# Performance work log

Measured on AMD Instinct MI355X. Metric: run time of the kernel, lower is better.

Reference implementation:

```python
import jax, jax.numpy as jnp
import numpy as np
import math

B, N, D = 16, 2048, 256

def setup_inputs() -> dict:
    key = jax.random.key(0)
    kq, kk, kv = jax.random.split(key, 3)
    query = jax.random.normal(kq, (B, N, D), dtype=jnp.float32)
    k = jax.random.normal(kk, (B, N, D), dtype=jnp.float32)
    value = jax.random.normal(kv, (B, D, N), dtype=jnp.float32)  # channel-first [B, d_v, N]
    return {"query": query, "key": k, "value": value, "mask": 0}

def reference(query, key, value, mask):
    d_k = query.shape[-1]
    scale = 1.0 / math.sqrt(d_k)
    # scores: [B, N, N]
    scores = jnp.einsum('bnd,bmd->bnm', query, key) * scale
    p_attn = jax.nn.softmax(scores, axis=-1)
    # mask is a static Python int flag gating dropout; mask=0 -> no dropout (deterministic reference)
    if mask:
        pass  # dropout intentionally disabled in deterministic reference
    # out = p_attn @ value^T  -> [B, N, d_v]; module returns out.transpose(-2,-1) -> [B, d_v, N]
    out_t = jnp.einsum('bnm,bdm->bdn', p_attn, value)
    return (out_t, p_attn)
```

## Files before the change

kernel.cpp:

```cpp
#include <hip/hip_runtime.h>
#include <hip/hip_bf16.h>


using bf16x8 = __attribute__((ext_vector_type(8))) short;
using f32x4  = __attribute__((ext_vector_type(4))) float;

__device__ __forceinline__ short f2bf(float f) {
    unsigned u = __float_as_uint(f);
    u += 0x7fffu + ((u >> 16) & 1u);
    return (short)(u >> 16);
}

__device__ __forceinline__ f32x4 mfma16(bf16x8 a, bf16x8 b, f32x4 c) {
    return __builtin_amdgcn_mfma_f32_16x16x32_bf16(a, b, c, 0, 0, 0);
}

#define AS1(p) ((const __attribute__((address_space(1))) void*)(p))
#define AS3(p) ((__attribute__((address_space(3))) void*)(p))

__global__ __launch_bounds__(256)
void convert_qkv(const float* __restrict__ Q, const float* __restrict__ K,
                 const float* __restrict__ V, short* __restrict__ Qb,
                 short* __restrict__ Kb, short* __restrict__ Vb, size_t n8)
{
    size_t i = (size_t)blockIdx.x * 256 + threadIdx.x;
    const float* src;
    short* dst;
    float scale = 1.0f;
    if (i < n8)            { src = Q;  dst = Qb; scale = 0.0625f; }
    else if (i < 2 * n8)   { i -= n8;      src = K; dst = Kb; }
    else                   { i -= 2 * n8;  src = V; dst = Vb; }
    const f32x4* s4 = (const f32x4*)src;
    f32x4 a = __builtin_nontemporal_load(s4 + i * 2);
    f32x4 b = __builtin_nontemporal_load(s4 + i * 2 + 1);
    bf16x8 v;
    v[0] = f2bf(a[0] * scale); v[1] = f2bf(a[1] * scale);
    v[2] = f2bf(a[2] * scale); v[3] = f2bf(a[3] * scale);
    v[4] = f2bf(b[0] * scale); v[5] = f2bf(b[1] * scale);
    v[6] = f2bf(b[2] * scale); v[7] = f2bf(b[3] * scale);
    *(bf16x8*)(dst + i * 8) = v;
}

__global__ __launch_bounds__(512, 2)
void fused_attn(const short* __restrict__ Qb, const short* __restrict__ Kb,
                const short* __restrict__ Vb, float* __restrict__ Pout,
                float* __restrict__ outT)
{
    __shared__ __align__(16) short Klds[2][64 * 256];
    __shared__ __align__(16) short Vlds[2][256 * 64];
    __shared__ __align__(16) short Plds[128 * 64];
    float* lpart = (float*)Plds;

    constexpr float LOG2E = 1.4426950408889634f;

    const unsigned g  = blockIdx.x;
    const unsigned wg = (g & 7) * 32 + (g >> 3);
    const int b  = (int)(wg >> 4);
    const int nb = (int)(wg & 15);

    const int tid  = threadIdx.x;
    const int lane = tid & 63;
    const int wave = tid >> 6;
    const int wn  = wave >> 1;
    const int wm  = wave & 1;
    const int l15 = lane & 15;
    const int l4  = lane >> 4;

    const short* Kbase = Kb + (size_t)b * (2048 * 256);
    const short* Vbase = Vb + (size_t)b * (256 * 2048);

    const short* Qp = Qb + ((size_t)b * 2048 + (size_t)nb * 128) * 256;
    bf16x8 qf[2][8];
#pragma unroll
    for (int mf = 0; mf < 2; mf++)
#pragma unroll
        for (int ks = 0; ks < 8; ks++)
            qf[mf][ks] = *(const bf16x8*)(
                Qp + (size_t)(wn * 32 + mf * 16 + l15) * 256 + ks * 32 + l4 * 8);

    auto stage_k = [&](int t, int buf) {
#pragma unroll
        for (int i = 0; i < 4; i++) {
            int ml = i * 16 + wave * 2 + (lane >> 5);
            int c  = lane & 31;
            int cs = (c & 24) | ((c ^ ml) & 7);
            __builtin_amdgcn_global_load_lds(
                AS1(Kbase + (size_t)(t * 64 + ml) * 256 + cs * 8),
                AS3(&Klds[buf][i * 4096 + wave * 512]), 16, 0, 0);
        }
    };
    auto stage_v = [&](int t, int buf) {
#pragma unroll
        for (int i = 0; i < 4; i++) {
            int d  = i * 64 + wave * 8 + (lane >> 3);
            int c  = lane & 7;
            int cs = c ^ (d & 7);
            __builtin_amdgcn_global_load_lds(
                AS1(Vbase + (size_t)d * 2048 + t * 64 + cs * 8),
                AS3(&Vlds[buf][i * 4096 + wave * 512]), 16, 0, 0);
        }
    };

    auto qkt = [&](int buf, f32x4 sacT[2][2]) {
#pragma unroll
        for (int ks = 0; ks < 8; ks++) {
            bf16x8 kf[2];
#pragma unroll
            for (int nf = 0; nf < 2; nf++) {
                int m  = wm * 32 + nf * 16 + l15;
                int ch = (ks * 4 + l4) ^ (m & 7);
                kf[nf] = *(const bf16x8*)((const char*)&Klds[buf][0] + m * 512 + ch * 16);
            }
#pragma unroll
            for (int mf = 0; mf < 2; mf++)
#pragma unroll
                for (int nf = 0; nf < 2; nf++)
                    sacT[mf][nf] = mfma16(kf[nf], qf[mf][ks], sacT[mf][nf]);
        }
    };

    float lacc[2] = {0.f, 0.f};
    stage_k(0, 0);
    for (int t = 0; t < 32; t++) {
        __syncthreads();
        if (t + 1 < 32) stage_k(t + 1, (t + 1) & 1);
        f32x4 sacT[2][2];
#pragma unroll
        for (int mf = 0; mf < 2; mf++)
#pragma unroll
            for (int nf = 0; nf < 2; nf++)
                sacT[mf][nf] = f32x4{0.f, 0.f, 0.f, 0.f};
        qkt(t & 1, sacT);
#pragma unroll
        for (int mf = 0; mf < 2; mf++)
#pragma unroll
            for (int nf = 0; nf < 2; nf++)
#pragma unroll
                for (int r = 0; r < 4; r++)
                    lacc[mf] += exp2f(sacT[mf][nf][r] * LOG2E);
    }
#pragma unroll
    for (int mf = 0; mf < 2; mf++) {
        lacc[mf] += __shfl_xor(lacc[mf], 16);
        lacc[mf] += __shfl_xor(lacc[mf], 32);
    }
    if (l4 == 0) {
        lpart[wave * 32 + 0 * 16 + l15] = lacc[0];
        lpart[wave * 32 + 1 * 16 + l15] = lacc[1];
    }
    __syncthreads();
    float rl[2];
#pragma unroll
    for (int mf = 0; mf < 2; mf++)
        rl[mf] = 1.0f / (lpart[(wn * 2 + 0) * 32 + mf * 16 + l15] +
                         lpart[(wn * 2 + 1) * 32 + mf * 16 + l15]);

    f32x4 oac[4][4];
#pragma unroll
    for (int i = 0; i < 4; i++)
#pragma unroll
        for (int j = 0; j < 4; j++)
            oac[i][j] = f32x4{0.f, 0.f, 0.f, 0.f};

    stage_k(0, 0);
    stage_v(0, 0);
    float* prow = Pout + ((size_t)b * 2048 + (size_t)nb * 128) * 2048;

    for (int t = 0; t < 32; t++) {
        __syncthreads();
        f32x4 sacT[2][2];
#pragma unroll
        for (int mf = 0; mf < 2; mf++)
#pragma unroll
            for (int nf = 0; nf < 2; nf++)
                sacT[mf][nf] = f32x4{0.f, 0.f, 0.f, 0.f};
        qkt(t & 1, sacT);

        f32x4 pv4[2][2];
#pragma unroll
        for (int mf = 0; mf < 2; mf++)
#pragma unroll
            for (int nf = 0; nf < 2; nf++) {
#pragma unroll
                for (int r = 0; r < 4; r++)
                    pv4[mf][nf][r] = exp2f(sacT[mf][nf][r] * LOG2E) * rl[mf];
                short4 ps;
                ps.x = f2bf(pv4[mf][nf][0]); ps.y = f2bf(pv4[mf][nf][1]);
                ps.z = f2bf(pv4[mf][nf][2]); ps.w = f2bf(pv4[mf][nf][3]);
                const int n  = wn * 32 + mf * 16 + l15;
                const int mb = wm * 32 + nf * 16 + l4 * 4;
                const int ch = (mb >> 3) ^ (n & 7);
                *(short4*)((char*)Plds + n * 128 + ch * 16 + (mb & 7) * 2) = ps;
            }
        __syncthreads();

        if (t + 1 < 32) {
            stage_k(t + 1, (t + 1) & 1);
            stage_v(t + 1, (t + 1) & 1);
        }

#pragma unroll
        for (int mf = 0; mf < 2; mf++)
#pragma unroll
            for (int nf = 0; nf < 2; nf++) {
                const int n  = wn * 32 + mf * 16 + l15;
                const int m  = t * 64 + wm * 32 + nf * 16 + l4 * 4;
                __builtin_nontemporal_store(pv4[mf][nf],
                    (f32x4*)(prow + (size_t)n * 2048 + m));
            }

        const char* vb_ = (const char*)&Vlds[t & 1][0];
#pragma unroll
        for (int ksl = 0; ksl < 2; ksl++) {
            bf16x8 vf[4], pf[4];
#pragma unroll
            for (int mf4 = 0; mf4 < 4; mf4++) {
                const int d  = wn * 64 + mf4 * 16 + l15;
                const int ch = (ksl * 4 + l4) ^ (d & 7);
                vf[mf4] = *(const bf16x8*)(vb_ + d * 128 + ch * 16);
            }
#pragma unroll
            for (int nf4 = 0; nf4 < 4; nf4++) {
                const int n  = wm * 64 + nf4 * 16 + l15;
                const int ch = (ksl * 4 + l4) ^ (n & 7);
                pf[nf4] = *(const bf16x8*)((const char*)Plds + n * 128 + ch * 16);
            }
#pragma unroll
            for (int mf4 = 0; mf4 < 4; mf4++)
#pragma unroll
                for (int nf4 = 0; nf4 < 4; nf4++)
                    oac[mf4][nf4] = mfma16(vf[mf4], pf[nf4], oac[mf4][nf4]);
        }
    }

    float* op = outT + (size_t)b * (256 * 2048) + (size_t)nb * 128;
#pragma unroll
    for (int mf4 = 0; mf4 < 4; mf4++)
#pragma unroll
        for (int nf4 = 0; nf4 < 4; nf4++)
#pragma unroll
            for (int r = 0; r < 4; r++) {
                int d = wn * 64 + mf4 * 16 + l4 * 4 + r;
                int n = wm * 64 + nf4 * 16 + l15;
                op[(size_t)d * 2048 + n] = oac[mf4][nf4][r];
            }
}

template<int BM, int BN, int BK>
__global__ __launch_bounds__(256)
void gemm_abt(const float* __restrict__ A, const float* __restrict__ B,
              float* __restrict__ C, int M, int N, int K,
              long strideA, long strideB, long strideC, float scale)
{
    const int b  = blockIdx.z;
    const int bm = blockIdx.y;
    const int bn = blockIdx.x;
    A += (size_t)b * strideA;
    B += (size_t)b * strideB;
    C += (size_t)b * strideC;

    constexpr int LDT = BK + 8;
    __shared__ __align__(16) short Alds[BM][LDT];
    __shared__ __align__(16) short Blds[BN][LDT];

    const int tid  = threadIdx.x;
    const int lane = tid & 63;
    const int wave = tid >> 6;
    const int wr   = wave >> 1;
    const int wc   = wave & 1;

    f32x4 acc[4][4];
#pragma unroll
    for (int m = 0; m < 4; m++)
#pragma unroll
        for (int n = 0; n < 4; n++)
            acc[m][n] = f32x4{0.f, 0.f, 0.f, 0.f};

    const float* Ab = A + (size_t)(bm * BM) * K;
    const float* Bb = B + (size_t)(bn * BN) * K;

    const int tr  = tid >> 4;
    const int tc4 = (tid & 15) << 2;

    for (int k0 = 0; k0 < K; k0 += BK) {
        __syncthreads();
#pragma unroll
        for (int r = tr; r < BM; r += 16) {
            const float4 v = *(const float4*)(Ab + (size_t)r * K + k0 + tc4);
            short4 s;
            s.x = f2bf(v.x); s.y = f2bf(v.y); s.z = f2bf(v.z); s.w = f2bf(v.w);
            *(short4*)&Alds[r][tc4] = s;
        }
#pragma unroll
        for (int r = tr; r < BN; r += 16) {
            const float4 v = *(const float4*)(Bb + (size_t)r * K + k0 + tc4);
            short4 s;
            s.x = f2bf(v.x); s.y = f2bf(v.y); s.z = f2bf(v.z); s.w = f2bf(v.w);
            *(short4*)&Blds[r][tc4] = s;
        }
        __syncthreads();

#pragma unroll
        for (int kk = 0; kk < BK; kk += 32) {
            const int ko = kk + ((lane >> 4) << 3);
            bf16x8 af[4], bfr[4];
#pragma unroll
            for (int m = 0; m < 4; m++)
                af[m] = *(const bf16x8*)&Alds[wr * 64 + m * 16 + (lane & 15)][ko];
#pragma unroll
            for (int n = 0; n < 4; n++)
                bfr[n] = *(const bf16x8*)&Blds[wc * 64 + n * 16 + (lane & 15)][ko];
#pragma unroll
            for (int m = 0; m < 4; m++)
#pragma unroll
                for (int n = 0; n < 4; n++)
                    acc[m][n] = __builtin_amdgcn_mfma_f32_16x16x32_bf16(
                        af[m], bfr[n], acc[m][n], 0, 0, 0);
        }
    }

    float* Cb = C + (size_t)(bm * BM) * N + (size_t)bn * BN;
    const int rbase = wr * 64 + ((lane >> 4) << 2);
    const int cbase = wc * 64 + (lane & 15);
#pragma unroll
    for (int m = 0; m < 4; m++)
#pragma unroll
        for (int n = 0; n < 4; n++)
#pragma unroll
            for (int r = 0; r < 4; r++)
                Cb[(size_t)(rbase + m * 16 + r) * N + cbase + n * 16] =
                    acc[m][n][r] * scale;
}

__global__ __launch_bounds__(256)
void softmax_rows(float* __restrict__ P)
{
    const size_t row = blockIdx.x;
    float* p = P + row * 2048;
    const int tid  = threadIdx.x;
    const int lane = tid & 63;
    const int wave = tid >> 6;

    float4 v0 = ((const float4*)p)[tid];
    float4 v1 = ((const float4*)p)[tid + 256];

    float m = fmaxf(fmaxf(fmaxf(v0.x, v0.y), fmaxf(v0.z, v0.w)),
                    fmaxf(fmaxf(v1.x, v1.y), fmaxf(v1.z, v1.w)));
#pragma unroll
    for (int off = 32; off; off >>= 1) m = fmaxf(m, __shfl_xor(m, off));

    __shared__ float sred[4];
    __shared__ float ssum[4];
    if (lane == 0) sred[wave] = m;
    __syncthreads();
    m = fmaxf(fmaxf(sred[0], sred[1]), fmaxf(sred[2], sred[3]));

    v0.x = expf(v0.x - m); v0.y = expf(v0.y - m);
    v0.z = expf(v0.z - m); v0.w = expf(v0.w - m);
    v1.x = expf(v1.x - m); v1.y = expf(v1.y - m);
    v1.z = expf(v1.z - m); v1.w = expf(v1.w - m);

    float s = (v0.x + v0.y + v0.z + v0.w) + (v1.x + v1.y + v1.z + v1.w);
#pragma unroll
    for (int off = 32; off; off >>= 1) s += __shfl_xor(s, off);
    if (lane == 0) ssum[wave] = s;
    __syncthreads();
    s = ssum[0] + ssum[1] + ssum[2] + ssum[3];

    const float r = 1.0f / s;
    v0.x *= r; v0.y *= r; v0.z *= r; v0.w *= r;
    v1.x *= r; v1.y *= r; v1.z *= r; v1.w *= r;

    ((float4*)p)[tid]       = v0;
    ((float4*)p)[tid + 256] = v1;
}

extern "C" void kernel_launch(void* const* d_in, const int* in_sizes, int n_in,
                              void* d_out, int out_size, void* d_ws, size_t ws_size,
                              hipStream_t stream)
{
    const float* Q  = (const float*)d_in[0];
    const float* Kk = (const float*)d_in[1];
    const float* V  = (const float*)d_in[2];

    float* outT = (float*)d_out;
    float* P    = outT + (size_t)16 * 256 * 2048;

    const size_t nQ = (size_t)16 * 2048 * 256;
    const long sQK = (long)2048 * 256;
    const long sP  = (long)2048 * 2048;
    const long sO  = (long)256 * 2048;

    const size_t needQKV = 3 * nQ * sizeof(short);

    if (ws_size >= needQKV) {
        short* Qb = (short*)d_ws;
        short* Kb = Qb + nQ;
        short* Vb = Kb + nQ;

        convert_qkv<<<dim3((unsigned)(3 * nQ / 8 / 256)), 256, 0, stream>>>(
            Q, Kk, V, Qb, Kb, Vb, nQ / 8);

        fused_attn<<<dim3(256), 512, 0, stream>>>(Qb, Kb, Vb, P, outT);
    } else {
        gemm_abt<128, 128, 64><<<dim3(16, 16, 16), 256, 0, stream>>>(
            Q, Kk, P, 2048, 2048, 256, sQK, sQK, sP, 0.0625f);
        softmax_rows<<<dim3(16 * 2048), 256, 0, stream>>>(P);
        gemm_abt<128, 128, 64><<<dim3(16, 2, 16), 256, 0, stream>>>(
            V, P, outT, 256, 2048, 2048, sO, sP, sO, 1.0f);
    }
}
```

Before: 185.1 us.

## Halve query tile to 64 rows, single-buffer V in LDS, raise occupancy

The fused attention kernel now gives each block 64 query rows instead of 128 and launches 512 blocks instead of 256. K and V are no longer double-buffered in the second pass; they share one LDS region, and launch bounds ask for 4 blocks per CU. Per-wave accumulators shrink, and s_setprio is raised around the MFMA sections. The aim is more resident waves and better CU fill for hiding latency, at the cost of recomputing QK^T for twice as many blocks, reloading K/V twice as often, and giving up load/compute overlap in the second pass.

```diff
diff --git a/kernel.cpp b/kernel.cpp
--- a/kernel.cpp
+++ b/kernel.cpp
@@ -41,35 +41,36 @@
     *(bf16x8*)(dst + i * 8) = v;
 }
 
-__global__ __launch_bounds__(512, 2)
+__global__ __launch_bounds__(512, 4)
 void fused_attn(const short* __restrict__ Qb, const short* __restrict__ Kb,
                 const short* __restrict__ Vb, float* __restrict__ Pout,
                 float* __restrict__ outT)
 {
-    __shared__ __align__(16) short Klds[2][64 * 256];
-    __shared__ __align__(16) short Vlds[2][256 * 64];
-    __shared__ __align__(16) short Plds[128 * 64];
+    __shared__ __align__(16) short Kl[2][64 * 256];
+    __shared__ __align__(16) short Plds[64 * 64];
     float* lpart = (float*)Plds;
 
     constexpr float LOG2E = 1.4426950408889634f;
 
     const unsigned g  = blockIdx.x;
-    const unsigned wg = (g & 7) * 32 + (g >> 3);
-    const int b  = (int)(wg >> 4);
-    const int nb = (int)(wg & 15);
+    const unsigned wg = (g & 7) * 64 + (g >> 3);
+    const int b  = (int)(wg >> 5);
+    const int nb = (int)(wg & 31);
 
     const int tid  = threadIdx.x;
     const int lane = tid & 63;
     const int wave = tid >> 6;
-    const int wn  = wave >> 1;
-    const int wm  = wave & 1;
     const int l15 = lane & 15;
     const int l4  = lane >> 4;
+    const int wn  = wave & 1;
+    const int wm  = wave >> 1;
+    const int nh  = wave & 1;
+    const int dq  = wave >> 1;
 
     const short* Kbase = Kb + (size_t)b * (2048 * 256);
     const short* Vbase = Vb + (size_t)b * (256 * 2048);
 
-    const short* Qp = Qb + ((size_t)b * 2048 + (size_t)nb * 128) * 256;
+    const short* Qp = Qb + ((size_t)b * 2048 + (size_t)nb * 64) * 256;
     bf16x8 qf[2][8];
 #pragma unroll
     for (int mf = 0; mf < 2; mf++)
@@ -86,10 +87,10 @@
             int cs = (c & 24) | ((c ^ ml) & 7);
             __builtin_amdgcn_global_load_lds(
                 AS1(Kbase + (size_t)(t * 64 + ml) * 256 + cs * 8),
-                AS3(&Klds[buf][i * 4096 + wave * 512]), 16, 0, 0);
+                AS3(&Kl[buf][i * 4096 + wave * 512]), 16, 0, 0);
         }
     };
-    auto stage_v = [&](int t, int buf) {
+    auto stage_v = [&](int t) {
 #pragma unroll
         for (int i = 0; i < 4; i++) {
             int d  = i * 64 + wave * 8 + (lane >> 3);
@@ -97,26 +98,22 @@
             int cs = c ^ (d & 7);
             __builtin_amdgcn_global_load_lds(
                 AS1(Vbase + (size_t)d * 2048 + t * 64 + cs * 8),
-                AS3(&Vlds[buf][i * 4096 + wave * 512]), 16, 0, 0);
+                AS3(&Kl[1][i * 4096 + wave * 512]), 16, 0, 0);
         }
     };
 
-    auto qkt = [&](int buf, f32x4 sacT[2][2]) {
+    auto qkt = [&](int buf, f32x4 sacT[2]) {
+        __builtin_amdgcn_s_setprio(1);
 #pragma unroll
         for (int ks = 0; ks < 8; ks++) {
-            bf16x8 kf[2];
-#pragma unroll
-            for (int nf = 0; nf < 2; nf++) {
-                int m  = wm * 32 + nf * 16 + l15;
-                int ch = (ks * 4 + l4) ^ (m & 7);
-                kf[nf] = *(const bf16x8*)((const char*)&Klds[buf][0] + m * 512 + ch * 16);
-            }
+            const int m  = wm * 16 + l15;
+            const int ch = (ks * 4 + l4) ^ (m & 7);
+            bf16x8 kf = *(const bf16x8*)((const char*)&Kl[buf][0] + m * 512 + ch * 16);
 #pragma unroll
             for (int mf = 0; mf < 2; mf++)
-#pragma unroll
-                for (int nf = 0; nf < 2; nf++)
-                    sacT[mf][nf] = mfma16(kf[nf], qf[mf][ks], sacT[mf][nf]);
-        }
+                sacT[mf] = mfma16(kf, qf[mf][ks], sacT[mf]);
+        }
+        __builtin_amdgcn_s_setprio(0);
     };
 
     float lacc[2] = {0.f, 0.f};
@@ -124,20 +121,15 @@
     for (int t = 0; t < 32; t++) {
         __syncthreads();
         if (t + 1 < 32) stage_k(t + 1, (t + 1) & 1);
-        f32x4 sacT[2][2];
+        f32x4 sacT[2];
+        sacT[0] = f32x4{0.f, 0.f, 0.f, 0.f};
+        sacT[1] = f32x4{0.f, 0.f, 0.f, 0.f};
+        qkt(t & 1, sacT);
 #pragma unroll
         for (int mf = 0; mf < 2; mf++)
 #pragma unroll
-            for (int nf = 0; nf < 2; nf++)
-                sacT[mf][nf] = f32x4{0.f, 0.f, 0.f, 0.f};
-        qkt(t & 1, sacT);
-#pragma unroll
-        for (int mf = 0; mf < 2; mf++)
-#pragma unroll
-            for (int nf = 0; nf < 2; nf++)
-#pragma unroll
-                for (int r = 0; r < 4; r++)
-                    lacc[mf] += exp2f(sacT[mf][nf][r] * LOG2E);
+            for (int r = 0; r < 4; r++)
+                lacc[mf] += exp2f(sacT[mf][r] * LOG2E);
     }
 #pragma unroll
     for (int mf = 0; mf < 2; mf++) {
@@ -151,98 +143,98 @@
     __syncthreads();
     float rl[2];
 #pragma unroll
-    for (int mf = 0; mf < 2; mf++)
-        rl[mf] = 1.0f / (lpart[(wn * 2 + 0) * 32 + mf * 16 + l15] +
-                         lpart[(wn * 2 + 1) * 32 + mf * 16 + l15]);
-
-    f32x4 oac[4][4];
+    for (int mf = 0; mf < 2; mf++) {
+        float s = 0.f;
+#pragma unroll
+        for (int w4 = 0; w4 < 4; w4++)
+            s += lpart[(w4 * 2 + wn) * 32 + mf * 16 + l15];
+        rl[mf] = 1.0f / s;
+    }
+    __syncthreads();
+
+    f32x4 oac[4][2];
 #pragma unroll
     for (int i = 0; i < 4; i++)
 #pragma unroll
-        for (int j = 0; j < 4; j++)
+        for (int j = 0; j < 2; j++)
             oac[i][j] = f32x4{0.f, 0.f, 0.f, 0.f};
 
     stage_k(0, 0);
-    stage_v(0, 0);
-    float* prow = Pout + ((size_t)b * 2048 + (size_t)nb * 128) * 2048;
+    stage_v(0);
+    float* prow = Pout + ((size_t)b * 2048 + (size_t)nb * 64) * 2048;
 
     for (int t = 0; t < 32; t++) {
         __syncthreads();
-        f32x4 sacT[2][2];
-#pragma unroll
-        for (int mf = 0; mf < 2; mf++)
-#pragma unroll
-            for (int nf = 0; nf < 2; nf++)
-                sacT[mf][nf] = f32x4{0.f, 0.f, 0.f, 0.f};
-        qkt(t & 1, sacT);
-
-        f32x4 pv4[2][2];
-#pragma unroll
-        for (int mf = 0; mf < 2; mf++)
-#pragma unroll
-            for (int nf = 0; nf < 2; nf++) {
-#pragma unroll
-                for (int r = 0; r < 4; r++)
-                    pv4[mf][nf][r] = exp2f(sacT[mf][nf][r] * LOG2E) * rl[mf];
-                short4 ps;
-                ps.x = f2bf(pv4[mf][nf][0]); ps.y = f2bf(pv4[mf][nf][1]);
-                ps.z = f2bf(pv4[mf][nf][2]); ps.w = f2bf(pv4[mf][nf][3]);
-                const int n  = wn * 32 + mf * 16 + l15;
-                const int mb = wm * 32 + nf * 16 + l4 * 4;
-                const int ch = (mb >> 3) ^ (n & 7);
-                *(short4*)((char*)Plds + n * 128 + ch * 16 + (mb & 7) * 2) = ps;
+        f32x4 sacT[2];
+        sacT[0] = f32x4{0.f, 0.f, 0.f, 0.f};
+        sacT[1] = f32x4{0.f, 0.f, 0.f, 0.f};
+        qkt(0, sacT);
+
+        f32x4 pv4[2];
+#pragma unroll
+        for (int mf = 0; mf < 2; mf++) {
+#pragma unroll
+            for (int r = 0; r < 4; r++)
+                pv4[mf][r] = exp2f(sacT[mf][r] * LOG2E) * rl[mf];
+            short4 ps;
+            ps.x = f2bf(pv4[mf][0]); ps.y = f2bf(pv4[mf][1]);
+            ps.z = f2bf(pv4[mf][2]); ps.w = f2bf(pv4[mf][3]);
+            const int n  = wn * 32 + mf * 16 + l15;
+            const int mb = wm * 16 + l4 * 4;
+            const int ch = (mb >> 3) ^ (n & 7);
+            *(short4*)((char*)Plds + n * 128 + ch * 16 + (mb & 7) * 2) = ps;
+        }
+        __syncthreads();
+
+#pragma unroll
+        for (int mf = 0; mf < 2; mf++) {
+            const int n = wn * 32 + mf * 16 + l15;
+            const int m = t * 64 + wm * 16 + l4 * 4;
+            __builtin_nontemporal_store(pv4[mf],
+                (f32x4*)(prow + (size_t)n * 2048 + m));
+        }
+
+        __builtin_amdgcn_s_setprio(1);
+#pragma unroll
+        for (int ksl = 0; ksl < 2; ksl++) {
+            bf16x8 vf[4], pf[2];
+#pragma unroll
+            for (int mf4 = 0; mf4 < 4; mf4++) {
+                const int d  = dq * 64 + mf4 * 16 + l15;
+                const int ch = (ksl * 4 + l4) ^ (d & 7);
+                vf[mf4] = *(const bf16x8*)((const char*)&Kl[1][0] + d * 128 + ch * 16);
             }
+#pragma unroll
+            for (int nf2 = 0; nf2 < 2; nf2++) {
+                const int n  = nh * 32 + nf2 * 16 + l15;
+                const int ch = (ksl * 4 + l4) ^ (n & 7);
+                pf[nf2] = *(const bf16x8*)((const char*)Plds + n * 128 + ch * 16);
+            }
+#pragma unroll
+            for (int mf4 = 0; mf4 < 4; mf4++)
+#pragma unroll
+                for (int nf2 = 0; nf2 < 2; nf2++)
+                    oac[mf4][nf2] = mfma16(vf[mf4], pf[nf2], oac[mf4][nf2]);
+        }
+        __builtin_amdgcn_s_setprio(0);
         __syncthreads();
 
         if (t + 1 < 32) {
-            stage_k(t + 1, (t + 1) & 1);
-            stage_v(t + 1, (t + 1) & 1);
-        }
-
-#pragma unroll
-        for (int mf = 0; mf < 2; mf++)
-#pragma unroll
-            for (int nf = 0; nf < 2; nf++) {
-                const int n  = wn * 32 + mf * 16 + l15;
-                const int m  = t * 64 + wm * 32 + nf * 16 + l4 * 4;
-                __builtin_nontemporal_store(pv4[mf][nf],
-                    (f32x4*)(prow + (size_t)n * 2048 + m));
-            }
-
-        const char* vb_ = (const char*)&Vlds[t & 1][0];
-#pragma unroll
-        for (int ksl = 0; ksl < 2; ksl++) {
-            bf16x8 vf[4], pf[4];
-#pragma unroll
-            for (int mf4 = 0; mf4 < 4; mf4++) {
-                const int d  = wn * 64 + mf4 * 16 + l15;
-                const int ch = (ksl * 4 + l4) ^ (d & 7);
-                vf[mf4] = *(const bf16x8*)(vb_ + d * 128 + ch * 16);
-            }
-#pragma unroll
-            for (int nf4 = 0; nf4 < 4; nf4++) {
-                const int n  = wm * 64 + nf4 * 16 + l15;
-                const int ch = (ksl * 4 + l4) ^ (n & 7);
-                pf[nf4] = *(const bf16x8*)((const char*)Plds + n * 128 + ch * 16);
-            }
-#pragma unroll
-            for (int mf4 = 0; mf4 < 4; mf4++)
-#pragma unroll
-                for (int nf4 = 0; nf4 < 4; nf4++)
-                    oac[mf4][nf4] = mfma16(vf[mf4], pf[nf4], oac[mf4][nf4]);
-        }
-    }
-
-    float* op = outT + (size_t)b * (256 * 2048) + (size_t)nb * 128;
+            stage_k(t + 1, 0);
+            stage_v(t + 1);
+        }
+    }
+
+    float* op = outT + (size_t)b * (256 * 2048) + (size_t)nb * 64;
 #pragma unroll
     for (int mf4 = 0; mf4 < 4; mf4++)
 #pragma unroll
-        for (int nf4 = 0; nf4 < 4; nf4++)
+        for (int nf2 = 0; nf2 < 2; nf2++)
 #pragma unroll
             for (int r = 0; r < 4; r++) {
-                int d = wn * 64 + mf4 * 16 + l4 * 4 + r;
-                int n = wm * 64 + nf4 * 16 + l15;
-                op[(size_t)d * 2048 + n] = oac[mf4][nf4][r];
+                int d = dq * 64 + mf4 * 16 + l4 * 4 + r;
+                int n = nh * 32 + nf2 * 16 + l15;
+                op[(size_t)d * 2048 + n] = oac[mf4][nf2][r];
             }
 }
 
@@ -401,7 +393,7 @@
         convert_qkv<<<dim3((unsigned)(3 * nQ / 8 / 256)), 256, 0, stream>>>(
             Q, Kk, V, Qb, Kb, Vb, nQ / 8);
 
-        fused_attn<<<dim3(256), 512, 0, stream>>>(Qb, Kb, Vb, P, outT);
+        fused_attn<<<dim3(512), 512, 0, stream>>>(Qb, Kb, Vb, P, outT);
     } else {
         gemm_abt<128, 128, 64><<<dim3(16, 16, 16), 256, 0, stream>>>(
             Q, Kk, P, 2048, 2048, 256, sQK, sQK, sP, 0.0625f);
```

Measured after the change: 380.7 us. +105.7%, slower.

## Warp-specialize attention: producer waves compute P, consumer waves do PV

Applied to the files above, without the earlier changes.

The second pass of the fused attention kernel is split by role. Waves 0-3 compute the QK^T tile, the softmax probabilities and the P global stores. Waves 4-7 run the P·V^T MFMAs for the previous tile, reading from a now double-buffered P in LDS, so only one barrier is needed per iteration. V staging is issued one step earlier, K for the second pass is prefetched during the normalizer reduction, and s_setprio raises wave priority around the MFMA loops. This aims to overlap the exp/store work with the PV matrix math, at the cost of 160KB of LDS, more accumulator registers in the consumer waves and a pipeline that can only go as fast as its slower half.

```diff
diff --git a/kernel.cpp b/kernel.cpp
--- a/kernel.cpp
+++ b/kernel.cpp
@@ -46,10 +46,10 @@
                 const short* __restrict__ Vb, float* __restrict__ Pout,
                 float* __restrict__ outT)
 {
-    __shared__ __align__(16) short Klds[2][64 * 256];
-    __shared__ __align__(16) short Vlds[2][256 * 64];
-    __shared__ __align__(16) short Plds[128 * 64];
-    float* lpart = (float*)Plds;
+    __shared__ __align__(16) short Kl[2][64 * 256];
+    __shared__ __align__(16) short Vl[2][256 * 64];
+    __shared__ __align__(16) short Pl[2][128 * 64];
+    float* lpart = (float*)Pl;
 
     constexpr float LOG2E = 1.4426950408889634f;
 
@@ -61,10 +61,9 @@
     const int tid  = threadIdx.x;
     const int lane = tid & 63;
     const int wave = tid >> 6;
-    const int wn  = wave >> 1;
-    const int wm  = wave & 1;
     const int l15 = lane & 15;
     const int l4  = lane >> 4;
+    const int qg  = wave & 3;
 
     const short* Kbase = Kb + (size_t)b * (2048 * 256);
     const short* Vbase = Vb + (size_t)b * (256 * 2048);
@@ -76,7 +75,7 @@
 #pragma unroll
         for (int ks = 0; ks < 8; ks++)
             qf[mf][ks] = *(const bf16x8*)(
-                Qp + (size_t)(wn * 32 + mf * 16 + l15) * 256 + ks * 32 + l4 * 8);
+                Qp + (size_t)(qg * 32 + mf * 16 + l15) * 256 + ks * 32 + l4 * 8);
 
     auto stage_k = [&](int t, int buf) {
 #pragma unroll
@@ -86,7 +85,7 @@
             int cs = (c & 24) | ((c ^ ml) & 7);
             __builtin_amdgcn_global_load_lds(
                 AS1(Kbase + (size_t)(t * 64 + ml) * 256 + cs * 8),
-                AS3(&Klds[buf][i * 4096 + wave * 512]), 16, 0, 0);
+                AS3(&Kl[buf][i * 4096 + wave * 512]), 16, 0, 0);
         }
     };
     auto stage_v = [&](int t, int buf) {
@@ -97,25 +96,7 @@
             int cs = c ^ (d & 7);
             __builtin_amdgcn_global_load_lds(
                 AS1(Vbase + (size_t)d * 2048 + t * 64 + cs * 8),
-                AS3(&Vlds[buf][i * 4096 + wave * 512]), 16, 0, 0);
-        }
-    };
-
-    auto qkt = [&](int buf, f32x4 sacT[2][2]) {
-#pragma unroll
-        for (int ks = 0; ks < 8; ks++) {
-            bf16x8 kf[2];
-#pragma unroll
-            for (int nf = 0; nf < 2; nf++) {
-                int m  = wm * 32 + nf * 16 + l15;
-                int ch = (ks * 4 + l4) ^ (m & 7);
-                kf[nf] = *(const bf16x8*)((const char*)&Klds[buf][0] + m * 512 + ch * 16);
-            }
-#pragma unroll
-            for (int mf = 0; mf < 2; mf++)
-#pragma unroll
-                for (int nf = 0; nf < 2; nf++)
-                    sacT[mf][nf] = mfma16(kf[nf], qf[mf][ks], sacT[mf][nf]);
+                AS3(&Vl[buf][i * 4096 + wave * 512]), 16, 0, 0);
         }
     };
 
@@ -124,13 +105,30 @@
     for (int t = 0; t < 32; t++) {
         __syncthreads();
         if (t + 1 < 32) stage_k(t + 1, (t + 1) & 1);
+        const char* kbuf = (const char*)&Kl[t & 1][0];
         f32x4 sacT[2][2];
 #pragma unroll
         for (int mf = 0; mf < 2; mf++)
 #pragma unroll
             for (int nf = 0; nf < 2; nf++)
                 sacT[mf][nf] = f32x4{0.f, 0.f, 0.f, 0.f};
-        qkt(t & 1, sacT);
+        __builtin_amdgcn_s_setprio(1);
+#pragma unroll
+        for (int ks = 0; ks < 8; ks++) {
+            bf16x8 kf[2];
+#pragma unroll
+            for (int nf = 0; nf < 2; nf++) {
+                int m  = (wave >> 2) * 32 + nf * 16 + l15;
+                int ch = (ks * 4 + l4) ^ (m & 7);
+                kf[nf] = *(const bf16x8*)(kbuf + m * 512 + ch * 16);
+            }
+#pragma unroll
+            for (int mf = 0; mf < 2; mf++)
+#pragma unroll
+                for (int nf = 0; nf < 2; nf++)
+                    sacT[mf][nf] = mfma16(kf[nf], qf[mf][ks], sacT[mf][nf]);
+        }
+        __builtin_amdgcn_s_setprio(0);
 #pragma unroll
         for (int mf = 0; mf < 2; mf++)
 #pragma unroll
@@ -139,6 +137,7 @@
                 for (int r = 0; r < 4; r++)
                     lacc[mf] += exp2f(sacT[mf][nf][r] * LOG2E);
     }
+    stage_k(0, 0);
 #pragma unroll
     for (int mf = 0; mf < 2; mf++) {
         lacc[mf] += __shfl_xor(lacc[mf], 16);
@@ -152,98 +151,114 @@
     float rl[2];
 #pragma unroll
     for (int mf = 0; mf < 2; mf++)
-        rl[mf] = 1.0f / (lpart[(wn * 2 + 0) * 32 + mf * 16 + l15] +
-                         lpart[(wn * 2 + 1) * 32 + mf * 16 + l15]);
-
-    f32x4 oac[4][4];
+        rl[mf] = 1.0f / (lpart[qg * 32 + mf * 16 + l15] +
+                         lpart[(qg + 4) * 32 + mf * 16 + l15]);
+    __syncthreads();
+
+    f32x4 oac[4][8];
 #pragma unroll
     for (int i = 0; i < 4; i++)
 #pragma unroll
-        for (int j = 0; j < 4; j++)
+        for (int j = 0; j < 8; j++)
             oac[i][j] = f32x4{0.f, 0.f, 0.f, 0.f};
 
-    stage_k(0, 0);
-    stage_v(0, 0);
     float* prow = Pout + ((size_t)b * 2048 + (size_t)nb * 128) * 2048;
+    const int cw = wave - 4;
+
+    auto consume = [&](int tt) {
+        const char* vbuf = (const char*)&Vl[tt & 1][0];
+        const char* pbuf = (const char*)&Pl[tt & 1][0];
+        __builtin_amdgcn_s_setprio(1);
+#pragma unroll
+        for (int ksl = 0; ksl < 2; ksl++) {
+            bf16x8 vf[4];
+#pragma unroll
+            for (int df = 0; df < 4; df++) {
+                int d  = cw * 64 + df * 16 + l15;
+                int ch = (ksl * 4 + l4) ^ (d & 7);
+                vf[df] = *(const bf16x8*)(vbuf + d * 128 + ch * 16);
+            }
+#pragma unroll
+            for (int nf = 0; nf < 8; nf++) {
+                int n  = nf * 16 + l15;
+                int ch = (ksl * 4 + l4) ^ (n & 7);
+                bf16x8 pf = *(const bf16x8*)(pbuf + n * 128 + ch * 16);
+#pragma unroll
+                for (int df = 0; df < 4; df++)
+                    oac[df][nf] = mfma16(vf[df], pf, oac[df][nf]);
+            }
+        }
+        __builtin_amdgcn_s_setprio(0);
+    };
 
     for (int t = 0; t < 32; t++) {
+        if (t + 1 < 32) stage_k(t + 1, (t + 1) & 1);
+        stage_v(t, t & 1);
+
+        if (wave < 4) {
+            const char* kbuf = (const char*)&Kl[t & 1][0];
+            f32x4 sacT[2][4];
+#pragma unroll
+            for (int mf = 0; mf < 2; mf++)
+#pragma unroll
+                for (int nf = 0; nf < 4; nf++)
+                    sacT[mf][nf] = f32x4{0.f, 0.f, 0.f, 0.f};
+            __builtin_amdgcn_s_setprio(1);
+#pragma unroll
+            for (int ks = 0; ks < 8; ks++) {
+                bf16x8 kf[4];
+#pragma unroll
+                for (int nf = 0; nf < 4; nf++) {
+                    int m  = nf * 16 + l15;
+                    int ch = (ks * 4 + l4) ^ (m & 7);
+                    kf[nf] = *(const bf16x8*)(kbuf + m * 512 + ch * 16);
+                }
+#pragma unroll
+                for (int mf = 0; mf < 2; mf++)
+#pragma unroll
+                    for (int nf = 0; nf < 4; nf++)
+                        sacT[mf][nf] = mfma16(kf[nf], qf[mf][ks], sacT[mf][nf]);
+            }
+            __builtin_amdgcn_s_setprio(0);
+
+            char* pw = (char*)&Pl[t & 1][0];
+#pragma unroll
+            for (int mf = 0; mf < 2; mf++)
+#pragma unroll
+                for (int nf = 0; nf < 4; nf++) {
+                    f32x4 pv4;
+#pragma unroll
+                    for (int r = 0; r < 4; r++)
+                        pv4[r] = exp2f(sacT[mf][nf][r] * LOG2E) * rl[mf];
+                    short4 ps;
+                    ps.x = f2bf(pv4[0]); ps.y = f2bf(pv4[1]);
+                    ps.z = f2bf(pv4[2]); ps.w = f2bf(pv4[3]);
+                    const int n  = qg * 32 + mf * 16 + l15;
+                    const int mb = nf * 16 + l4 * 4;
+                    const int ch = (mb >> 3) ^ (n & 7);
+                    *(short4*)(pw + n * 128 + ch * 16 + (mb & 7) * 2) = ps;
+                    __builtin_nontemporal_store(pv4,
+                        (f32x4*)(prow + (size_t)n * 2048 + t * 64 + mb));
+                }
+        } else if (t > 0) {
+            consume(t - 1);
+        }
         __syncthreads();
-        f32x4 sacT[2][2];
-#pragma unroll
-        for (int mf = 0; mf < 2; mf++)
-#pragma unroll
-            for (int nf = 0; nf < 2; nf++)
-                sacT[mf][nf] = f32x4{0.f, 0.f, 0.f, 0.f};
-        qkt(t & 1, sacT);
-
-        f32x4 pv4[2][2];
-#pragma unroll
-        for (int mf = 0; mf < 2; mf++)
-#pragma unroll
-            for (int nf = 0; nf < 2; nf++) {
-#pragma unroll
-                for (int r = 0; r < 4; r++)
-                    pv4[mf][nf][r] = exp2f(sacT[mf][nf][r] * LOG2E) * rl[mf];
-                short4 ps;
-                ps.x = f2bf(pv4[mf][nf][0]); ps.y = f2bf(pv4[mf][nf][1]);
-                ps.z = f2bf(pv4[mf][nf][2]); ps.w = f2bf(pv4[mf][nf][3]);
-                const int n  = wn * 32 + mf * 16 + l15;
-                const int mb = wm * 32 + nf * 16 + l4 * 4;
-                const int ch = (mb >> 3) ^ (n & 7);
-                *(short4*)((char*)Plds + n * 128 + ch * 16 + (mb & 7) * 2) = ps;
-            }
-        __syncthreads();
-
-        if (t + 1 < 32) {
-            stage_k(t + 1, (t + 1) & 1);
-            stage_v(t + 1, (t + 1) & 1);
-        }
-
-#pragma unroll
-        for (int mf = 0; mf < 2; mf++)
-#pragma unroll
-            for (int nf = 0; nf < 2; nf++) {
-                const int n  = wn * 32 + mf * 16 + l15;
-                const int m  = t * 64 + wm * 32 + nf * 16 + l4 * 4;
-                __builtin_nontemporal_store(pv4[mf][nf],
-                    (f32x4*)(prow + (size_t)n * 2048 + m));
-            }
-
-        const char* vb_ = (const char*)&Vlds[t & 1][0];
-#pragma unroll
-        for (int ksl = 0; ksl < 2; ksl++) {
-            bf16x8 vf[4], pf[4];
-#pragma unroll
-            for (int mf4 = 0; mf4 < 4; mf4++) {
-                const int d  = wn * 64 + mf4 * 16 + l15;
-                const int ch = (ksl * 4 + l4) ^ (d & 7);
-                vf[mf4] = *(const bf16x8*)(vb_ + d * 128 + ch * 16);
-            }
-#pragma unroll
-            for (int nf4 = 0; nf4 < 4; nf4++) {
-                const int n  = wm * 64 + nf4 * 16 + l15;
-                const int ch = (ksl * 4 + l4) ^ (n & 7);
-                pf[nf4] = *(const bf16x8*)((const char*)Plds + n * 128 + ch * 16);
-            }
-#pragma unroll
-            for (int mf4 = 0; mf4 < 4; mf4++)
-#pragma unroll
-                for (int nf4 = 0; nf4 < 4; nf4++)
-                    oac[mf4][nf4] = mfma16(vf[mf4], pf[nf4], oac[mf4][nf4]);
-        }
-    }
-
-    float* op = outT + (size_t)b * (256 * 2048) + (size_t)nb * 128;
-#pragma unroll
-    for (int mf4 = 0; mf4 < 4; mf4++)
-#pragma unroll
-        for (int nf4 = 0; nf4 < 4; nf4++)
-#pragma unroll
-            for (int r = 0; r < 4; r++) {
-                int d = wn * 64 + mf4 * 16 + l4 * 4 + r;
-                int n = wm * 64 + nf4 * 16 + l15;
-                op[(size_t)d * 2048 + n] = oac[mf4][nf4][r];
-            }
+    }
+    if (wave >= 4) {
+        consume(31);
+        float* op = outT + (size_t)b * (256 * 2048) + (size_t)nb * 128;
+#pragma unroll
+        for (int df = 0; df < 4; df++)
+#pragma unroll
+            for (int nf = 0; nf < 8; nf++)
+#pragma unroll
+                for (int r = 0; r < 4; r++) {
+                    int d = cw * 64 + df * 16 + l4 * 4 + r;
+                    int n = nf * 16 + l15;
+                    op[(size_t)d * 2048 + n] = oac[df][nf][r];
+                }
+    }
 }
 
 template<int BM, int BN, int BK>
```

Result: slower. 224.9 us (+21.5%).

## Split fused attention into a score GEMM and a fused softmax-PV kernel

Applied to the files above, without the earlier changes.

Replaces the single fused attention kernel, when workspace allows, with two kernels. The first is a tiled QK^T GEMM that stores bf16 scores and per-tile partial exp row sums. The second reads the scores, forms normalized probabilities, writes P, and multiplies by V with double-buffered LDS staging. This removes the in-kernel recomputation and serial dependency of the fused softmax and gives the GEMM much more parallelism, at the cost of a large bf16 score round trip through memory. The softmax skips max subtraction, which assumes the scaled scores stay small enough not to overflow exp.

```diff
diff --git a/kernel.cpp b/kernel.cpp
--- a/kernel.cpp
+++ b/kernel.cpp
@@ -10,13 +10,17 @@
     u += 0x7fffu + ((u >> 16) & 1u);
     return (short)(u >> 16);
 }
-
+__device__ __forceinline__ float bf2f(short s) {
+    return __uint_as_float(((unsigned)(unsigned short)s) << 16);
+}
 __device__ __forceinline__ f32x4 mfma16(bf16x8 a, bf16x8 b, f32x4 c) {
     return __builtin_amdgcn_mfma_f32_16x16x32_bf16(a, b, c, 0, 0, 0);
 }
 
 #define AS1(p) ((const __attribute__((address_space(1))) void*)(p))
 #define AS3(p) ((__attribute__((address_space(3))) void*)(p))
+
+constexpr float LOG2E = 1.4426950408889634f;
 
 __global__ __launch_bounds__(256)
 void convert_qkv(const float* __restrict__ Q, const float* __restrict__ K,
@@ -41,6 +45,247 @@
     *(bf16x8*)(dst + i * 8) = v;
 }
 
+__global__ __launch_bounds__(256)
+void gemm_s_lp(const short* __restrict__ A, const short* __restrict__ B,
+               short* __restrict__ Sb, float* __restrict__ lp)
+{
+    constexpr int BK = 64;
+    const unsigned g  = blockIdx.x;
+    const unsigned wg = (g & 7) * 512 + (g >> 3);
+    const int bn = (int)(wg & 15);
+    const int bm = (int)((wg >> 4) & 15);
+    const int b  = (int)(wg >> 8);
+
+    const short* Ab = A + (size_t)b * (2048 * 256) + (size_t)(bm * 128) * 256;
+    const short* Bb = B + (size_t)b * (2048 * 256) + (size_t)(bn * 128) * 256;
+
+    __shared__ __align__(16) short Alds[128 * BK];
+    __shared__ __align__(16) short Blds[128 * BK];
+    __shared__ float lred[2][128];
+
+    const int tid  = threadIdx.x;
+    const int lane = tid & 63;
+    const int wave = tid >> 6;
+    const int wr   = wave >> 1;
+    const int wc   = wave & 1;
+    const int l15  = lane & 15;
+    const int l4   = lane >> 4;
+
+    f32x4 acc[4][4];
+#pragma unroll
+    for (int m = 0; m < 4; m++)
+#pragma unroll
+        for (int n = 0; n < 4; n++)
+            acc[m][n] = f32x4{0.f, 0.f, 0.f, 0.f};
+
+    const int r0 = wave * 8 + (lane >> 3);
+    const int c0 = (lane & 7) * 8;
+
+    for (int k0 = 0; k0 < 256; k0 += BK) {
+        __syncthreads();
+#pragma unroll
+        for (int i = 0; i < 4; i++)
+            __builtin_amdgcn_global_load_lds(
+                AS1(Ab + (size_t)(i * 32 + r0) * 256 + k0 + c0),
+                AS3(Alds + i * 2048 + wave * 512), 16, 0, 0);
+#pragma unroll
+        for (int i = 0; i < 4; i++)
+            __builtin_amdgcn_global_load_lds(
+                AS1(Bb + (size_t)(i * 32 + r0) * 256 + k0 + c0),
+                AS3(Blds + i * 2048 + wave * 512), 16, 0, 0);
+        __syncthreads();
+
+#pragma unroll
+        for (int kk = 0; kk < BK; kk += 32) {
+            const int ko = kk + (l4 << 3);
+            bf16x8 af[4], bfr[4];
+#pragma unroll
+            for (int m = 0; m < 4; m++)
+                af[m] = *(const bf16x8*)&Alds[(wr * 64 + m * 16 + l15) * BK + ko];
+#pragma unroll
+            for (int n = 0; n < 4; n++)
+                bfr[n] = *(const bf16x8*)&Blds[(wc * 64 + n * 16 + l15) * BK + ko];
+#pragma unroll
+            for (int m = 0; m < 4; m++)
+#pragma unroll
+                for (int n = 0; n < 4; n++)
+                    acc[m][n] = mfma16(af[m], bfr[n], acc[m][n]);
+        }
+    }
+
+    short* Cb = Sb + (size_t)b * (2048UL * 2048) + (size_t)(bm * 128) * 2048
+              + (size_t)bn * 128;
+    const int rbase = wr * 64 + (l4 << 2);
+    const int cbase = wc * 64 + l15;
+    float esum[4][4];
+#pragma unroll
+    for (int m = 0; m < 4; m++)
+#pragma unroll
+        for (int r = 0; r < 4; r++)
+            esum[m][r] = 0.f;
+#pragma unroll
+    for (int m = 0; m < 4; m++)
+#pragma unroll
+        for (int n = 0; n < 4; n++)
+#pragma unroll
+            for (int r = 0; r < 4; r++) {
+                const short sv = f2bf(acc[m][n][r]);
+                Cb[(size_t)(rbase + m * 16 + r) * 2048 + cbase + n * 16] = sv;
+                esum[m][r] += exp2f(bf2f(sv) * LOG2E);
+            }
+#pragma unroll
+    for (int dlt = 1; dlt < 16; dlt <<= 1)
+#pragma unroll
+        for (int m = 0; m < 4; m++)
+#pragma unroll
+            for (int r = 0; r < 4; r++)
+                esum[m][r] += __shfl_xor(esum[m][r], dlt);
+    if (l15 == 0)
+#pragma unroll
+        for (int m = 0; m < 4; m++)
+#pragma unroll
+            for (int r = 0; r < 4; r++)
+                lred[wc][rbase + m * 16 + r] = esum[m][r];
+    __syncthreads();
+    if (tid < 128)
+        lp[((size_t)b * 2048 + bm * 128 + tid) * 16 + bn] =
+            lred[0][tid] + lred[1][tid];
+}
+
+__global__ __launch_bounds__(512, 2)
+void pv_attn(const short* __restrict__ Sb, const short* __restrict__ Vb,
+             const float* __restrict__ lp, float* __restrict__ Pout,
+             float* __restrict__ outT)
+{
+    __shared__ __align__(16) short Sl[2][128 * 64];
+    __shared__ __align__(16) short Vl[2][256 * 64];
+
+    const unsigned g  = blockIdx.x;
+    const unsigned wg = (g & 7) * 32 + (g >> 3);
+    const int b  = (int)(wg >> 4);
+    const int nb = (int)(wg & 15);
+
+    const int tid  = threadIdx.x;
+    const int lane = tid & 63;
+    const int wave = tid >> 6;
+    const int l15  = lane & 15;
+    const int l4   = lane >> 4;
+
+    const short* Sbase = Sb + ((size_t)b * 2048 + (size_t)nb * 128) * 2048;
+    const short* Vbase = Vb + (size_t)b * (256 * 2048);
+
+    const int nmine = tid >> 2;
+    const int mseg  = tid & 3;
+    const f32x4* lp4 = (const f32x4*)(lp + ((size_t)b * 2048 + nb * 128 + nmine) * 16);
+    float ls = 0.f;
+#pragma unroll
+    for (int j = 0; j < 4; j++) {
+        const f32x4 lv = lp4[j];
+        ls += lv[0] + lv[1] + lv[2] + lv[3];
+    }
+    const float rlmine = 1.0f / ls;
+    float* prow_mine = Pout + ((size_t)b * 2048 + (size_t)nb * 128 + nmine) * 2048;
+
+    auto stage_s = [&](int t, int buf) {
+#pragma unroll
+        for (int i = 0; i < 2; i++) {
+            int ri = i * 64 + wave * 8 + (lane >> 3);
+            int c  = lane & 7;
+            int cs = c ^ (ri & 7);
+            __builtin_amdgcn_global_load_lds(
+                AS1(Sbase + (size_t)ri * 2048 + t * 64 + cs * 8),
+                AS3(&Sl[buf][i * 4096 + wave * 512]), 16, 0, 0);
+        }
+    };
+    auto stage_v = [&](int t, int buf) {
+#pragma unroll
+        for (int i = 0; i < 4; i++) {
+            int d  = i * 64 + wave * 8 + (lane >> 3);
+            int c  = lane & 7;
+            int cs = c ^ (d & 7);
+            __builtin_amdgcn_global_load_lds(
+                AS1(Vbase + (size_t)d * 2048 + t * 64 + cs * 8),
+                AS3(&Vl[buf][i * 4096 + wave * 512]), 16, 0, 0);
+        }
+    };
+
+    f32x4 oac[2][8];
+#pragma unroll
+    for (int i = 0; i < 2; i++)
+#pragma unroll
+        for (int j = 0; j < 8; j++)
+            oac[i][j] = f32x4{0.f, 0.f, 0.f, 0.f};
+
+    stage_s(0, 0);
+    stage_v(0, 0);
+
+    const int ch0 = (mseg * 2) ^ (nmine & 7);
+    const int ch1 = (mseg * 2 + 1) ^ (nmine & 7);
+
+    for (int t = 0; t < 32; t++) {
+        __syncthreads();
+
+        char* sbuf = (char*)&Sl[t & 1][0];
+        bf16x8 s0 = *(bf16x8*)(sbuf + nmine * 128 + ch0 * 16);
+        bf16x8 s1 = *(bf16x8*)(sbuf + nmine * 128 + ch1 * 16);
+        float p[16];
+#pragma unroll
+        for (int j = 0; j < 8; j++) {
+            p[j]     = exp2f(bf2f(s0[j]) * LOG2E) * rlmine;
+            p[8 + j] = exp2f(bf2f(s1[j]) * LOG2E) * rlmine;
+        }
+        bf16x8 o0, o1;
+#pragma unroll
+        for (int j = 0; j < 8; j++) { o0[j] = f2bf(p[j]); o1[j] = f2bf(p[8 + j]); }
+        *(bf16x8*)(sbuf + nmine * 128 + ch0 * 16) = o0;
+        *(bf16x8*)(sbuf + nmine * 128 + ch1 * 16) = o1;
+        __syncthreads();
+
+        float* pd = prow_mine + t * 64 + mseg * 16;
+        __builtin_nontemporal_store(f32x4{p[0],  p[1],  p[2],  p[3]},  (f32x4*)pd);
+        __builtin_nontemporal_store(f32x4{p[4],  p[5],  p[6],  p[7]},  (f32x4*)(pd + 4));
+        __builtin_nontemporal_store(f32x4{p[8],  p[9],  p[10], p[11]}, (f32x4*)(pd + 8));
+        __builtin_nontemporal_store(f32x4{p[12], p[13], p[14], p[15]}, (f32x4*)(pd + 12));
+        if (t + 1 < 32) { stage_s(t + 1, (t + 1) & 1); stage_v(t + 1, (t + 1) & 1); }
+
+        const char* vbuf = (const char*)&Vl[t & 1][0];
+        const char* pbuf = (const char*)&Sl[t & 1][0];
+        __builtin_amdgcn_s_setprio(1);
+#pragma unroll
+        for (int ksl = 0; ksl < 2; ksl++) {
+            bf16x8 vf[2];
+#pragma unroll
+            for (int df = 0; df < 2; df++) {
+                int d  = wave * 32 + df * 16 + l15;
+                int ch = (ksl * 4 + l4) ^ (d & 7);
+                vf[df] = *(const bf16x8*)(vbuf + d * 128 + ch * 16);
+            }
+#pragma unroll
+            for (int nf = 0; nf < 8; nf++) {
+                int n  = nf * 16 + l15;
+                int ch = (ksl * 4 + l4) ^ (n & 7);
+                bf16x8 pf = *(const bf16x8*)(pbuf + n * 128 + ch * 16);
+#pragma unroll
+                for (int df = 0; df < 2; df++)
+                    oac[df][nf] = mfma16(vf[df], pf, oac[df][nf]);
+            }
+        }
+        __builtin_amdgcn_s_setprio(0);
+    }
+
+    float* op = outT + (size_t)b * (256 * 2048) + (size_t)nb * 128;
+#pragma unroll
+    for (int df = 0; df < 2; df++)
+#pragma unroll
+        for (int nf = 0; nf < 8; nf++)
+#pragma unroll
+            for (int r = 0; r < 4; r++) {
+                int d = wave * 32 + df * 16 + l4 * 4 + r;
+                int n = nf * 16 + l15;
+                op[(size_t)d * 2048 + n] = oac[df][nf][r];
+            }
+}
+
 __global__ __launch_bounds__(512, 2)
 void fused_attn(const short* __restrict__ Qb, const short* __restrict__ Kb,
                 const short* __restrict__ Vb, float* __restrict__ Pout,
@@ -51,8 +296,6 @@
     __shared__ __align__(16) short Plds[128 * 64];
     float* lpart = (float*)Plds;
 
-    constexpr float LOG2E = 1.4426950408889634f;
-
     const unsigned g  = blockIdx.x;
     const unsigned wg = (g & 7) * 32 + (g >> 3);
     const int b  = (int)(wg >> 4);
@@ -100,7 +343,6 @@
                 AS3(&Vlds[buf][i * 4096 + wave * 512]), 16, 0, 0);
         }
     };
-
     auto qkt = [&](int buf, f32x4 sacT[2][2]) {
 #pragma unroll
         for (int ks = 0; ks < 8; ks++) {
@@ -387,11 +629,14 @@
     float* P    = outT + (size_t)16 * 256 * 2048;
 
     const size_t nQ = (size_t)16 * 2048 * 256;
+    const size_t nP = (size_t)16 * 2048 * 2048;
     const long sQK = (long)2048 * 256;
     const long sP  = (long)2048 * 2048;
     const long sO  = (long)256 * 2048;
 
-    const size_t needQKV = 3 * nQ * sizeof(short);
+    const size_t needQKV   = 3 * nQ * sizeof(short);
+    const size_t lpBytes   = (size_t)16 * 2048 * 16 * sizeof(float);
+    const size_t needSplit = needQKV + lpBytes + nP * sizeof(short);
 
     if (ws_size >= needQKV) {
         short* Qb = (short*)d_ws;
@@ -401,7 +646,14 @@
         convert_qkv<<<dim3((unsigned)(3 * nQ / 8 / 256)), 256, 0, stream>>>(
             Q, Kk, V, Qb, Kb, Vb, nQ / 8);
 
-        fused_attn<<<dim3(256), 512, 0, stream>>>(Qb, Kb, Vb, P, outT);
+        if (ws_size >= needSplit) {
+            float* lp = (float*)(Vb + nQ);
+            short* Sb = (short*)(lp + (size_t)16 * 2048 * 16);
+            gemm_s_lp<<<dim3(4096), 256, 0, stream>>>(Qb, Kb, Sb, lp);
+            pv_attn<<<dim3(256), 512, 0, stream>>>(Sb, Vb, lp, P, outT);
+        } else {
+            fused_attn<<<dim3(256), 512, 0, stream>>>(Qb, Kb, Vb, P, outT);
+        }
     } else {
         gemm_abt<128, 128, 64><<<dim3(16, 16, 16), 256, 0, stream>>>(
             Q, Kk, P, 2048, 2048, 256, sQK, sQK, sP, 0.0625f);
```

Result: slower. 327.0 us (+76.6%).
